# Kernel tuning notes

Hardware: AMD Instinct MI355X
Metric: run time of the kernel (lower is better)

## Reference

```python
import jax, jax.numpy as jnp
import numpy as np

L_PREDS = 2
BATCH = 256
PNUM = 512


def setup_inputs() -> dict:
    key = jax.random.key(0)
    k1, k2 = jax.random.split(key)
    pred_list = jax.random.normal(k1, (L_PREDS, BATCH, PNUM, 2), dtype=jnp.float32)
    gt = jax.random.normal(k2, (BATCH, PNUM, 2), dtype=jnp.float32)
    return {"pred_list": pred_list, "gt": gt}


def _smooth_l1(x):
    # F.smooth_l1_loss with default beta=1.0, reduction='none'
    ax = jnp.abs(x)
    return jnp.where(ax < 1.0, 0.5 * x * x, ax - 0.5)


def _match_loss(pred, gt):
    # pred, gt: [B, pnum, 2]
    pnum = pred.shape[1]
    # idx[i, j] = (j + i) % pnum  -> cyclic rotation i of the gt polygon
    idx = (jnp.arange(pnum)[:, None] + jnp.arange(pnum)[None, :]) % pnum  # [pnum, pnum]
    gt_expand = gt[:, idx, :]                      # [B, pnum(rot), pnum(pt), 2]
    diff = _smooth_l1(pred[:, None, :, :] - gt_expand)
    dis = diff.sum(-1).mean(-1)                    # [B, pnum(rot)]
    return jnp.min(dis, axis=1)                    # [B] : best rotation per sample


def reference(pred_list, gt):
    n = pred_list.shape[0]
    loss = jnp.float32(0.0)
    for i in range(n):  # small fixed number of prediction stages
        loss = loss + jnp.mean(_match_loss(pred_list[i], gt))
    return loss / n
```

## Files before the change

kernel.cpp:

```cpp
#include <hip/hip_runtime.h>

#define PNUM 512
#define LB_BLOCKS 512

__global__ __launch_bounds__(512)
void poly_match_kernel(const float* __restrict__ pred,
                       const float* __restrict__ gt,
                       float* __restrict__ block_min)
{
    __shared__ float2 sp[PNUM];
    __shared__ float2 sg2[2 * PNUM];
    __shared__ float swave[8];

    const int bid = blockIdx.x;
    const int b   = bid & 255;
    const int t   = threadIdx.x;

    const float2* pp = (const float2*)(pred + (size_t)bid * PNUM * 2);
    const float2* gp = (const float2*)(gt   + (size_t)b   * PNUM * 2);

    float2 g = gp[t];
    sp[t]          = pp[t];
    sg2[t]         = g;
    sg2[t + PNUM]  = g;
    __syncthreads();

    const int i = t;
    float acc = 0.0f;

    #pragma unroll 8
    for (int j = 0; j < PNUM; ++j) {
        float2 p  = sp[j];
        float2 gg = sg2[i + j];
        float dx = p.x - gg.x;
        float dy = p.y - gg.y;
        float ax = fabsf(dx);
        float ay = fabsf(dy);
        float tx = fminf(ax, 1.0f);
        float ty = fminf(ay, 1.0f);
        acc = fmaf(tx, fmaf(-0.5f, tx, ax), acc);
        acc = fmaf(ty, fmaf(-0.5f, ty, ay), acc);
    }

    float m = acc;
    #pragma unroll
    for (int d = 1; d < 64; d <<= 1)
        m = fminf(m, __shfl_xor(m, d, 64));

    const int lane = t & 63;
    const int w    = t >> 6;
    if (lane == 0) swave[w] = m;
    __syncthreads();
    if (t == 0) {
        float mm = swave[0];
        #pragma unroll
        for (int k = 1; k < 8; ++k) mm = fminf(mm, swave[k]);
        block_min[bid] = mm;
    }
}

__global__ __launch_bounds__(512)
void poly_match_finalize(const float* __restrict__ block_min,
                         float* __restrict__ out)
{
    const int t = threadIdx.x;
    float v = block_min[t];
    #pragma unroll
    for (int d = 1; d < 64; d <<= 1)
        v += __shfl_xor(v, d, 64);

    __shared__ float s[8];
    if ((t & 63) == 0) s[t >> 6] = v;
    __syncthreads();
    if (t == 0) {
        float tot = 0.0f;
        #pragma unroll
        for (int k = 0; k < 8; ++k) tot += s[k];
        out[0] = tot * (1.0f / (512.0f * 512.0f));
    }
}

extern "C" void kernel_launch(void* const* d_in, const int* in_sizes, int n_in,
                              void* d_out, int out_size, void* d_ws, size_t ws_size,
                              hipStream_t stream)
{
    const float* pred = (const float*)d_in[0];
    const float* gt   = (const float*)d_in[1];
    float* out  = (float*)d_out;
    float* bmin = (float*)d_ws;

    poly_match_kernel<<<LB_BLOCKS, PNUM, 0, stream>>>(pred, gt, bmin);
    poly_match_finalize<<<1, PNUM, 0, stream>>>(bmin, out);
}
```

Measured before the change: 83.10 us.

## Compute two rotations per thread with float4 shared-memory register reuse

Each thread now evaluates two adjacent cyclic rotations using float4 loads of prediction and ground-truth pairs, carrying the next gt vector in a register across iterations. Blocks shrink to 256 threads. This cuts LDS load instructions per computed term so the loop is less bound by shared memory. It trades fewer waves per block for more registers and ILP per thread.

Measured after the change: 96.97 us. +16.7%, slower.

```diff
diff --git a/kernel.cpp b/kernel.cpp
--- a/kernel.cpp
+++ b/kernel.cpp
@@ -3,58 +3,74 @@
 #define PNUM 512
 #define LB_BLOCKS 512
 
-__global__ __launch_bounds__(512)
+__global__ __launch_bounds__(256)
 void poly_match_kernel(const float* __restrict__ pred,
                        const float* __restrict__ gt,
                        float* __restrict__ block_min)
 {
-    __shared__ float2 sp[PNUM];
-    __shared__ float2 sg2[2 * PNUM];
-    __shared__ float swave[8];
+    __shared__ float4 sp4[PNUM / 2];
+    __shared__ float4 sg4[PNUM];
+    __shared__ float swave[4];
 
     const int bid = blockIdx.x;
     const int b   = bid & 255;
     const int t   = threadIdx.x;
 
-    const float2* pp = (const float2*)(pred + (size_t)bid * PNUM * 2);
-    const float2* gp = (const float2*)(gt   + (size_t)b   * PNUM * 2);
+    const float4* pp4 = (const float4*)(pred + (size_t)bid * PNUM * 2);
+    const float4* gp4 = (const float4*)(gt   + (size_t)b   * PNUM * 2);
 
-    float2 g = gp[t];
-    sp[t]          = pp[t];
-    sg2[t]         = g;
-    sg2[t + PNUM]  = g;
+    float4 gv = gp4[t];
+    sp4[t]        = pp4[t];
+    sg4[t]        = gv;
+    sg4[t + 256]  = gv;
     __syncthreads();
 
-    const int i = t;
-    float acc = 0.0f;
+    float acc0 = 0.0f, acc1 = 0.0f;
+
+    float4 W0 = sg4[t];
 
     #pragma unroll 8
-    for (int j = 0; j < PNUM; ++j) {
-        float2 p  = sp[j];
-        float2 gg = sg2[i + j];
-        float dx = p.x - gg.x;
-        float dy = p.y - gg.y;
-        float ax = fabsf(dx);
-        float ay = fabsf(dy);
-        float tx = fminf(ax, 1.0f);
-        float ty = fminf(ay, 1.0f);
-        acc = fmaf(tx, fmaf(-0.5f, tx, ax), acc);
-        acc = fmaf(ty, fmaf(-0.5f, ty, ay), acc);
+    for (int jj = 0; jj < 256; ++jj) {
+        const float4 P  = sp4[jj];
+        const float4 W1 = sg4[t + jj + 1];
+
+        {
+            float dx = P.x - W0.x, dy = P.y - W0.y;
+            float tx = fminf(fabsf(dx), 1.0f), ty = fminf(fabsf(dy), 1.0f);
+            acc0 = fmaf(tx, fmaf(-0.5f, tx, fabsf(dx)), acc0);
+            acc0 = fmaf(ty, fmaf(-0.5f, ty, fabsf(dy)), acc0);
+        }
+        {
+            float dx = P.z - W0.z, dy = P.w - W0.w;
+            float tx = fminf(fabsf(dx), 1.0f), ty = fminf(fabsf(dy), 1.0f);
+            acc0 = fmaf(tx, fmaf(-0.5f, tx, fabsf(dx)), acc0);
+            acc0 = fmaf(ty, fmaf(-0.5f, ty, fabsf(dy)), acc0);
+        }
+        {
+            float dx = P.x - W0.z, dy = P.y - W0.w;
+            float tx = fminf(fabsf(dx), 1.0f), ty = fminf(fabsf(dy), 1.0f);
+            acc1 = fmaf(tx, fmaf(-0.5f, tx, fabsf(dx)), acc1);
+            acc1 = fmaf(ty, fmaf(-0.5f, ty, fabsf(dy)), acc1);
+        }
+        {
+            float dx = P.z - W1.x, dy = P.w - W1.y;
+            float tx = fminf(fabsf(dx), 1.0f), ty = fminf(fabsf(dy), 1.0f);
+            acc1 = fmaf(tx, fmaf(-0.5f, tx, fabsf(dx)), acc1);
+            acc1 = fmaf(ty, fmaf(-0.5f, ty, fabsf(dy)), acc1);
+        }
+
+        W0 = W1;
     }
 
-    float m = acc;
+    float m = fminf(acc0, acc1);
     #pragma unroll
     for (int d = 1; d < 64; d <<= 1)
         m = fminf(m, __shfl_xor(m, d, 64));
 
-    const int lane = t & 63;
-    const int w    = t >> 6;
-    if (lane == 0) swave[w] = m;
+    if ((t & 63) == 0) swave[t >> 6] = m;
     __syncthreads();
     if (t == 0) {
-        float mm = swave[0];
-        #pragma unroll
-        for (int k = 1; k < 8; ++k) mm = fminf(mm, swave[k]);
+        float mm = fminf(fminf(swave[0], swave[1]), fminf(swave[2], swave[3]));
         block_min[bid] = mm;
     }
 }
@@ -89,6 +105,6 @@
     float* out  = (float*)d_out;
     float* bmin = (float*)d_ws;
 
-    poly_match_kernel<<<LB_BLOCKS, PNUM, 0, stream>>>(pred, gt, bmin);
+    poly_match_kernel<<<LB_BLOCKS, 256, 0, stream>>>(pred, gt, bmin);
     poly_match_finalize<<<1, PNUM, 0, stream>>>(bmin, out);
 }
```

## Split point loop into chunks with register-blocked rotations and a combine pass

Applied to the files above, without the earlier changes.

Each block now handles a quarter of the point dimension for one (stage, sample) pair. Every thread computes four rotations at once, keeping a sliding window of gt points in registers so each LDS read is reused across several rotations. Partial sums go to workspace and a new combine kernel sums the chunks and takes the min per sample. This aims to cut LDS traffic per FLOP and raise parallelism, at the cost of an extra kernel launch and a global round-trip for the partial sums.

Result: slower. 91.88 us (+10.6%).

```diff
diff --git a/kernel.cpp b/kernel.cpp
--- a/kernel.cpp
+++ b/kernel.cpp
@@ -1,70 +1,120 @@
 #include <hip/hip_runtime.h>
 
-#define PNUM 512
-#define LB_BLOCKS 512
+#define PNUM   512
+#define LB     512
+#define NCHUNK 4
+#define JCHUNK 128
+#define NSS    32
+
+#define SL1(px, py, qx, qy, accA, accB) {                        \
+    float dx_ = (px) - (qx), dy_ = (py) - (qy);                  \
+    float tx_ = fminf(fabsf(dx_), 1.0f);                         \
+    float ty_ = fminf(fabsf(dy_), 1.0f);                         \
+    accA = fmaf(tx_, fmaf(-0.5f, tx_, fabsf(dx_)), accA);        \
+    accB = fmaf(ty_, fmaf(-0.5f, ty_, fabsf(dy_)), accB); }
+
+#define BODY(P, W0, W1, W2)                                      \
+    SL1((P).x, (P).y, (W0).x, (W0).y, a0, b0);                   \
+    SL1((P).z, (P).w, (W0).z, (W0).w, a0, b0);                   \
+    SL1((P).x, (P).y, (W0).z, (W0).w, a1, b1);                   \
+    SL1((P).z, (P).w, (W1).x, (W1).y, a1, b1);                   \
+    SL1((P).x, (P).y, (W1).x, (W1).y, a2, b2);                   \
+    SL1((P).z, (P).w, (W1).z, (W1).w, a2, b2);                   \
+    SL1((P).x, (P).y, (W1).z, (W1).w, a3, b3);                   \
+    SL1((P).z, (P).w, (W2).x, (W2).y, a3, b3);
+
+__global__ __launch_bounds__(128, 4)
+void poly_partial_kernel(const float* __restrict__ pred,
+                         const float* __restrict__ gt,
+                         float* __restrict__ partial)
+{
+    __shared__ float4 sgE[260];
+    __shared__ float4 sgO[260];
+    __shared__ float4 spc[66];
+
+    const int bid   = blockIdx.x;
+    const int chunk = bid & 3;
+    const int lb    = bid >> 2;
+    const int b     = lb & 255;
+    const int t     = threadIdx.x;
+
+    const int KC = chunk * (JCHUNK / 2);
+    const int KH = KC >> 1;
+
+    const float4* pp4 = (const float4*)(pred + (size_t)lb * PNUM * 2);
+    const float4* gp4 = (const float4*)(gt   + (size_t)b  * PNUM * 2);
+
+    float4 ge = gp4[2 * t];
+    float4 go = gp4[2 * t + 1];
+    sgE[t]       = ge;  sgE[t + 128] = ge;
+    sgO[t]       = go;  sgO[t + 128] = go;
+    if (t < 4) { sgE[256 + t] = ge; sgO[256 + t] = go; }
+    if (t < 64)  spc[t] = pp4[KC + t];
+    if (t < 2)   spc[64 + t] = pp4[KC];
+    __syncthreads();
+
+    float a0 = 0.f, a1 = 0.f, a2 = 0.f, a3 = 0.f;
+    float b0 = 0.f, b1 = 0.f, b2 = 0.f, b3 = 0.f;
+
+    const int i0 = t + KH;
+    float4 W0 = sgE[i0];
+    float4 W1 = sgO[i0];
+    float4 W2 = sgE[i0 + 1];
+    float4 P  = spc[0];
+
+    #pragma unroll 4
+    for (int ss = 0; ss < NSS; ++ss) {
+        {
+            const float4 Wn = sgO[i0 + ss + 1];
+            const float4 Pn = spc[2 * ss + 1];
+            BODY(P, W0, W1, W2)
+            W0 = W1; W1 = W2; W2 = Wn; P = Pn;
+        }
+        {
+            const float4 Wn = sgE[i0 + ss + 2];
+            const float4 Pn = spc[2 * ss + 2];
+            BODY(P, W0, W1, W2)
+            W0 = W1; W1 = W2; W2 = Wn; P = Pn;
+        }
+    }
+
+    float4 r = make_float4(a0 + b0, a1 + b1, a2 + b2, a3 + b3);
+    ((float4*)partial)[(chunk * LB + lb) * 128 + t] = r;
+}
 
 __global__ __launch_bounds__(512)
-void poly_match_kernel(const float* __restrict__ pred,
-                       const float* __restrict__ gt,
-                       float* __restrict__ block_min)
+void poly_combine_kernel(const float* __restrict__ partial,
+                         float* __restrict__ bmin)
 {
-    __shared__ float2 sp[PNUM];
-    __shared__ float2 sg2[2 * PNUM];
-    __shared__ float swave[8];
+    const int lb = blockIdx.x;
+    const int t  = threadIdx.x;
 
-    const int bid = blockIdx.x;
-    const int b   = bid & 255;
-    const int t   = threadIdx.x;
+    float v = partial[(0 * LB + lb) * PNUM + t]
+            + partial[(1 * LB + lb) * PNUM + t]
+            + partial[(2 * LB + lb) * PNUM + t]
+            + partial[(3 * LB + lb) * PNUM + t];
 
-    const float2* pp = (const float2*)(pred + (size_t)bid * PNUM * 2);
-    const float2* gp = (const float2*)(gt   + (size_t)b   * PNUM * 2);
-
-    float2 g = gp[t];
-    sp[t]          = pp[t];
-    sg2[t]         = g;
-    sg2[t + PNUM]  = g;
-    __syncthreads();
-
-    const int i = t;
-    float acc = 0.0f;
-
-    #pragma unroll 8
-    for (int j = 0; j < PNUM; ++j) {
-        float2 p  = sp[j];
-        float2 gg = sg2[i + j];
-        float dx = p.x - gg.x;
-        float dy = p.y - gg.y;
-        float ax = fabsf(dx);
-        float ay = fabsf(dy);
-        float tx = fminf(ax, 1.0f);
-        float ty = fminf(ay, 1.0f);
-        acc = fmaf(tx, fmaf(-0.5f, tx, ax), acc);
-        acc = fmaf(ty, fmaf(-0.5f, ty, ay), acc);
-    }
-
-    float m = acc;
     #pragma unroll
     for (int d = 1; d < 64; d <<= 1)
-        m = fminf(m, __shfl_xor(m, d, 64));
+        v = fminf(v, __shfl_xor(v, d, 64));
 
-    const int lane = t & 63;
-    const int w    = t >> 6;
-    if (lane == 0) swave[w] = m;
+    __shared__ float s[8];
+    if ((t & 63) == 0) s[t >> 6] = v;
     __syncthreads();
     if (t == 0) {
-        float mm = swave[0];
+        float mm = s[0];
         #pragma unroll
-        for (int k = 1; k < 8; ++k) mm = fminf(mm, swave[k]);
-        block_min[bid] = mm;
+        for (int k = 1; k < 8; ++k) mm = fminf(mm, s[k]);
+        bmin[lb] = mm;
     }
 }
 
 __global__ __launch_bounds__(512)
-void poly_match_finalize(const float* __restrict__ block_min,
+void poly_match_finalize(const float* __restrict__ bmin,
                          float* __restrict__ out)
 {
     const int t = threadIdx.x;
-    float v = block_min[t];
+    float v = bmin[t];
     #pragma unroll
     for (int d = 1; d < 64; d <<= 1)
         v += __shfl_xor(v, d, 64);
@@ -86,9 +136,11 @@
 {
     const float* pred = (const float*)d_in[0];
     const float* gt   = (const float*)d_in[1];
-    float* out  = (float*)d_out;
-    float* bmin = (float*)d_ws;
+    float* out     = (float*)d_out;
+    float* partial = (float*)d_ws;
+    float* bmin    = (float*)d_ws + NCHUNK * LB * PNUM;
 
-    poly_match_kernel<<<LB_BLOCKS, PNUM, 0, stream>>>(pred, gt, bmin);
+    poly_partial_kernel<<<NCHUNK * LB, 128, 0, stream>>>(pred, gt, partial);
+    poly_combine_kernel<<<LB, PNUM, 0, stream>>>(partial, bmin);
     poly_match_finalize<<<1, PNUM, 0, stream>>>(bmin, out);
 }
```

## Register-tile rotations per thread and split points across waves for LDS reuse

Applied to the files above, without the earlier changes.

Each thread now accumulates eight rotations at once from a sliding window of float4 gt values held in registers, and each wave covers a 64-point slice of the polygon. Per-rotation partial sums are combined through shared memory before the min reduction. The aim is to cut LDS loads per smooth-L1 evaluation and use vectorised float4 LDS reads in place of the one-rotation-per-thread loop. The cost is higher register pressure and an extra shared-memory reduction stage with its barrier.

Measured after the change: 86.70 us. 4.3% more time.

```diff
diff --git a/kernel.cpp b/kernel.cpp
--- a/kernel.cpp
+++ b/kernel.cpp
@@ -1,70 +1,131 @@
 #include <hip/hip_runtime.h>
 
 #define PNUM 512
-#define LB_BLOCKS 512
+#define LB   512
 
-__global__ __launch_bounds__(512)
+#define SL1(px, py, qx, qy, accA, accB) {                        \
+    float dx_ = (px) - (qx), dy_ = (py) - (qy);                  \
+    float tx_ = fminf(fabsf(dx_), 1.0f);                         \
+    float ty_ = fminf(fabsf(dy_), 1.0f);                         \
+    accA = fmaf(tx_, fmaf(-0.5f, tx_, fabsf(dx_)), accA);        \
+    accB = fmaf(ty_, fmaf(-0.5f, ty_, fabsf(dy_)), accB); }
+
+#define BODY(Pv, W0, W1, W2, W3, W4)                             \
+    SL1((Pv).x,(Pv).y,(W0).x,(W0).y,a0,b0);                      \
+    SL1((Pv).z,(Pv).w,(W0).z,(W0).w,a0,b0);                      \
+    SL1((Pv).x,(Pv).y,(W0).z,(W0).w,a1,b1);                      \
+    SL1((Pv).z,(Pv).w,(W1).x,(W1).y,a1,b1);                      \
+    SL1((Pv).x,(Pv).y,(W1).x,(W1).y,a2,b2);                      \
+    SL1((Pv).z,(Pv).w,(W1).z,(W1).w,a2,b2);                      \
+    SL1((Pv).x,(Pv).y,(W1).z,(W1).w,a3,b3);                      \
+    SL1((Pv).z,(Pv).w,(W2).x,(W2).y,a3,b3);                      \
+    SL1((Pv).x,(Pv).y,(W2).x,(W2).y,a4,b4);                      \
+    SL1((Pv).z,(Pv).w,(W2).z,(W2).w,a4,b4);                      \
+    SL1((Pv).x,(Pv).y,(W2).z,(W2).w,a5,b5);                      \
+    SL1((Pv).z,(Pv).w,(W3).x,(W3).y,a5,b5);                      \
+    SL1((Pv).x,(Pv).y,(W3).x,(W3).y,a6,b6);                      \
+    SL1((Pv).z,(Pv).w,(W3).z,(W3).w,a6,b6);                      \
+    SL1((Pv).x,(Pv).y,(W3).z,(W3).w,a7,b7);                      \
+    SL1((Pv).z,(Pv).w,(W4).x,(W4).y,a7,b7);
+
+__global__ __launch_bounds__(512, 4)
 void poly_match_kernel(const float* __restrict__ pred,
                        const float* __restrict__ gt,
-                       float* __restrict__ block_min)
+                       float* __restrict__ bmin)
 {
-    __shared__ float2 sp[PNUM];
-    __shared__ float2 sg2[2 * PNUM];
-    __shared__ float swave[8];
+    __shared__ float4 sg[4][132];
+    __shared__ float4 spred[258];
+    __shared__ float  part2[64][64];
+    __shared__ float  swave[8];
 
-    const int bid = blockIdx.x;
-    const int b   = bid & 255;
-    const int t   = threadIdx.x;
+    const int lb = blockIdx.x;
+    const int b  = lb & 255;
+    const int t  = threadIdx.x;
+    const int w  = t >> 6;
+    const int l  = t & 63;
 
-    const float2* pp = (const float2*)(pred + (size_t)bid * PNUM * 2);
-    const float2* gp = (const float2*)(gt   + (size_t)b   * PNUM * 2);
+    const float4* pp4 = (const float4*)(pred + (size_t)lb * PNUM * 2);
+    const float4* gp4 = (const float4*)(gt   + (size_t)b  * PNUM * 2);
 
-    float2 g = gp[t];
-    sp[t]          = pp[t];
-    sg2[t]         = g;
-    sg2[t + PNUM]  = g;
+    sg[t & 3][t >> 2] = gp4[t & 255];
+    if (t < 8)   sg[t & 3][128 + (t >> 2)] = gp4[t];
+    if (t < 256) spred[t] = pp4[t];
+    if (t == 0)  spred[256] = pp4[0];
     __syncthreads();
 
-    const int i = t;
-    float acc = 0.0f;
+    const int A  = l + 8 * w;
+    const int pb = 32 * w;
 
-    #pragma unroll 8
-    for (int j = 0; j < PNUM; ++j) {
-        float2 p  = sp[j];
-        float2 gg = sg2[i + j];
-        float dx = p.x - gg.x;
-        float dy = p.y - gg.y;
-        float ax = fabsf(dx);
-        float ay = fabsf(dy);
-        float tx = fminf(ax, 1.0f);
-        float ty = fminf(ay, 1.0f);
-        acc = fmaf(tx, fmaf(-0.5f, tx, ax), acc);
-        acc = fmaf(ty, fmaf(-0.5f, ty, ay), acc);
+    float a0=0.f,a1=0.f,a2=0.f,a3=0.f,a4=0.f,a5=0.f,a6=0.f,a7=0.f;
+    float b0=0.f,b1=0.f,b2=0.f,b3=0.f,b4=0.f,b5=0.f,b6=0.f,b7=0.f;
+
+    float4 v0 = sg[0][A];
+    float4 v1 = sg[1][A];
+    float4 v2 = sg[2][A];
+    float4 v3 = sg[3][A];
+    float4 v4 = sg[0][A + 1];
+    float4 P  = spred[pb];
+
+    for (int q = 0; q < 8; ++q) {
+        const float4 n0  = sg[1][A + q + 1];
+        const float4 Pn  = spred[pb + 4 * q + 1];
+        BODY(P, v0, v1, v2, v3, v4)
+
+        const float4 n1  = sg[2][A + q + 1];
+        const float4 Pn2 = spred[pb + 4 * q + 2];
+        BODY(Pn, v1, v2, v3, v4, n0)
+
+        const float4 n2  = sg[3][A + q + 1];
+        const float4 Pn3 = spred[pb + 4 * q + 3];
+        BODY(Pn2, v2, v3, v4, n0, n1)
+
+        const float4 n3  = sg[0][A + q + 2];
+        const float4 Pn4 = spred[pb + 4 * q + 4];
+        BODY(Pn3, v3, v4, n0, n1, n2)
+
+        v0 = v4; v1 = n0; v2 = n1; v3 = n2; v4 = n3; P = Pn4;
     }
 
-    float m = acc;
-    #pragma unroll
-    for (int d = 1; d < 64; d <<= 1)
-        m = fminf(m, __shfl_xor(m, d, 64));
+    part2[w * 8 + 0][l] = a0 + b0;
+    part2[w * 8 + 1][l] = a1 + b1;
+    part2[w * 8 + 2][l] = a2 + b2;
+    part2[w * 8 + 3][l] = a3 + b3;
+    part2[w * 8 + 4][l] = a4 + b4;
+    part2[w * 8 + 5][l] = a5 + b5;
+    part2[w * 8 + 6][l] = a6 + b6;
+    part2[w * 8 + 7][l] = a7 + b7;
+    __syncthreads();
 
-    const int lane = t & 63;
-    const int w    = t >> 6;
-    if (lane == 0) swave[w] = m;
-    __syncthreads();
-    if (t == 0) {
-        float mm = swave[0];
+    {
+        const int g  = t >> 6;
+        const int l2 = t & 63;
+        float v = part2[g][l2];
         #pragma unroll
-        for (int k = 1; k < 8; ++k) mm = fminf(mm, swave[k]);
-        block_min[bid] = mm;
+        for (int ww = 1; ww < 8; ++ww)
+            v += part2[ww * 8 + g][l2];
+
+        float m = v;
+        #pragma unroll
+        for (int d = 1; d < 64; d <<= 1)
+            m = fminf(m, __shfl_xor(m, d, 64));
+
+        if (l2 == 0) swave[g] = m;
+        __syncthreads();
+        if (t == 0) {
+            float mm = swave[0];
+            #pragma unroll
+            for (int k = 1; k < 8; ++k) mm = fminf(mm, swave[k]);
+            bmin[lb] = mm;
+        }
     }
 }
 
 __global__ __launch_bounds__(512)
-void poly_match_finalize(const float* __restrict__ block_min,
+void poly_match_finalize(const float* __restrict__ bmin,
                          float* __restrict__ out)
 {
     const int t = threadIdx.x;
-    float v = block_min[t];
+    float v = bmin[t];
     #pragma unroll
     for (int d = 1; d < 64; d <<= 1)
         v += __shfl_xor(v, d, 64);
@@ -89,6 +150,6 @@
     float* out  = (float*)d_out;
     float* bmin = (float*)d_ws;
 
-    poly_match_kernel<<<LB_BLOCKS, PNUM, 0, stream>>>(pred, gt, bmin);
+    poly_match_kernel<<<LB, 512, 0, stream>>>(pred, gt, bmin);
     poly_match_finalize<<<1, PNUM, 0, stream>>>(bmin, out);
 }
```
